# Performance work log

Hardware: AMD Instinct MI355X
Metric: run time of the kernel (lower is better)

Reference implementation:

```python
import jax, jax.numpy as jnp
import numpy as np


def setup_inputs() -> dict:
    key = jax.random.key(0)
    k1, k2 = jax.random.split(key)
    T, H, E = 16384, 4096, 8
    x = jax.random.normal(k1, (T, H), dtype=jnp.float32)
    W = jax.random.normal(k2, (E, H), dtype=jnp.float32) * 0.02  # torch Linear weight [out, in]
    return {"x": x, "W": W, "top_k": 2}


def reference(x, W, top_k):
    # router_logits = x @ W^T : [T, E]
    logits = jnp.einsum("th,eh->te", x, W)
    scores = jax.nn.softmax(logits.astype(jnp.float32), axis=-1)
    expert_weights, expert_indices = jax.lax.top_k(scores, top_k)
    return scores, expert_weights, expert_indices.astype(jnp.int32)
```

## Files before the change

### kernel.cpp

```cpp
#include <hip/hip_runtime.h>


#define ROUTER_H4 1024
#define ROUTER_E 8
#define ROWS_PER_WAVE 4
#define CHUNK 512
#define NCHUNK (ROUTER_H4 / CHUNK)

__global__ __launch_bounds__(1024) void learned_router_kernel(
    const float* __restrict__ x, const float* __restrict__ W,
    float* __restrict__ out_scores, float* __restrict__ out_w,
    float* __restrict__ out_idx, int n_rows)
{
    __shared__ float4 wlds[ROUTER_E][CHUNK];

    const int tid  = (int)threadIdx.x;
    const int wv   = tid >> 6;
    const int lane = tid & 63;
    const int row0 = (int)blockIdx.x * (16 * ROWS_PER_WAVE) + wv * ROWS_PER_WAVE;

    const float4* __restrict__ x4 = (const float4*)x;
    const float4* __restrict__ W4 = (const float4*)W;

    float acc[ROWS_PER_WAVE][ROUTER_E];
#pragma unroll
    for (int r = 0; r < ROWS_PER_WAVE; ++r)
#pragma unroll
        for (int e = 0; e < ROUTER_E; ++e) acc[r][e] = 0.f;

    for (int c = 0; c < NCHUNK; ++c) {
#pragma unroll
        for (int k = 0; k < 4; ++k) {
            const int flat = k * 1024 + tid;
            const int e    = flat >> 9;
            const int pos  = flat & (CHUNK - 1);
            wlds[e][pos] = W4[e * ROUTER_H4 + c * CHUNK + pos];
        }
        __syncthreads();

#pragma unroll 2
        for (int inner = 0; inner < CHUNK / 64; ++inner) {
            const int idx  = inner * 64 + lane;
            const int hpos = c * CHUNK + idx;
            float4 xv[ROWS_PER_WAVE];
#pragma unroll
            for (int r = 0; r < ROWS_PER_WAVE; ++r)
                xv[r] = x4[(size_t)(row0 + r) * ROUTER_H4 + hpos];
#pragma unroll
            for (int e = 0; e < ROUTER_E; ++e) {
                const float4 w4 = wlds[e][idx];
#pragma unroll
                for (int r = 0; r < ROWS_PER_WAVE; ++r)
                    acc[r][e] += xv[r].x * w4.x + xv[r].y * w4.y
                               + xv[r].z * w4.z + xv[r].w * w4.w;
            }
        }
        __syncthreads();
    }

#pragma unroll
    for (int off = 32; off > 0; off >>= 1) {
#pragma unroll
        for (int r = 0; r < ROWS_PER_WAVE; ++r)
#pragma unroll
            for (int e = 0; e < ROUTER_E; ++e)
                acc[r][e] += __shfl_xor(acc[r][e], off, 64);
    }

    if (lane == 0) {
#pragma unroll
        for (int r = 0; r < ROWS_PER_WAVE; ++r) {
            const int row = row0 + r;
            float m = acc[r][0];
#pragma unroll
            for (int e = 1; e < ROUTER_E; ++e) m = fmaxf(m, acc[r][e]);
            float p[ROUTER_E];
            float s = 0.f;
#pragma unroll
            for (int e = 0; e < ROUTER_E; ++e) { p[e] = __expf(acc[r][e] - m); s += p[e]; }
            const float inv = 1.f / s;
#pragma unroll
            for (int e = 0; e < ROUTER_E; ++e) p[e] *= inv;

            float4* os = (float4*)(out_scores + (size_t)row * ROUTER_E);
            os[0] = make_float4(p[0], p[1], p[2], p[3]);
            os[1] = make_float4(p[4], p[5], p[6], p[7]);

            int i0 = 0;
#pragma unroll
            for (int e = 1; e < ROUTER_E; ++e) if (p[e] > p[i0]) i0 = e;
            int i1 = (i0 == 0) ? 1 : 0;
#pragma unroll
            for (int e = 0; e < ROUTER_E; ++e) if (e != i0 && p[e] > p[i1]) i1 = e;

            *(float2*)(out_w + (size_t)row * 2)   = make_float2(p[i0], p[i1]);
            *(float2*)(out_idx + (size_t)row * 2) = make_float2((float)i0, (float)i1);
        }
    }
}

extern "C" void kernel_launch(void* const* d_in, const int* in_sizes, int n_in,
                              void* d_out, int out_size, void* d_ws, size_t ws_size,
                              hipStream_t stream) {
    const float* x = (const float*)d_in[0];
    const float* W = (const float*)d_in[1];
    const int T = in_sizes[0] / (ROUTER_H4 * 4);
    (void)n_in; (void)d_ws; (void)ws_size; (void)out_size;

    float* out = (float*)d_out;
    float* out_scores = out;
    float* out_w   = out + (size_t)T * ROUTER_E;
    float* out_idx = out_w + (size_t)T * 2;

    const int rows_per_block = 16 * ROWS_PER_WAVE;
    const int grid = (T + rows_per_block - 1) / rows_per_block;
    learned_router_kernel<<<grid, 1024, 0, stream>>>(x, W, out_scores, out_w, out_idx, T);
}
```

Before: 370.8 us.

## Stage full router weight in LDS once and double-buffer x loads per row pair

The kernel now loads all of W (128 KB) into shared memory in a single pass, which removes the per-chunk reload and the barriers inside the main loop. Each wave handles its four rows as two pairs. For each pair it prefetches the next group of four float4 x values while computing on the current group, a software double-buffering scheme meant to hide global-memory latency. The trade-offs are higher LDS use per block and fewer rows in flight per wave, which may lower memory-level parallelism.

Result: slower. 553.5 us (+49.3%).

```diff
diff --git a/kernel.cpp b/kernel.cpp
--- a/kernel.cpp
+++ b/kernel.cpp
@@ -3,98 +3,111 @@
 
 #define ROUTER_H4 1024
 #define ROUTER_E 8
-#define ROWS_PER_WAVE 4
-#define CHUNK 512
-#define NCHUNK (ROUTER_H4 / CHUNK)
 
 __global__ __launch_bounds__(1024) void learned_router_kernel(
     const float* __restrict__ x, const float* __restrict__ W,
     float* __restrict__ out_scores, float* __restrict__ out_w,
     float* __restrict__ out_idx, int n_rows)
 {
-    __shared__ float4 wlds[ROUTER_E][CHUNK];
+    __shared__ float4 wlds[ROUTER_E][ROUTER_H4];
 
     const int tid  = (int)threadIdx.x;
     const int wv   = tid >> 6;
     const int lane = tid & 63;
-    const int row0 = (int)blockIdx.x * (16 * ROWS_PER_WAVE) + wv * ROWS_PER_WAVE;
 
     const float4* __restrict__ x4 = (const float4*)x;
     const float4* __restrict__ W4 = (const float4*)W;
 
-    float acc[ROWS_PER_WAVE][ROUTER_E];
 #pragma unroll
-    for (int r = 0; r < ROWS_PER_WAVE; ++r)
+    for (int k = 0; k < 8; ++k) {
+        const int flat = k * 1024 + tid;
+        wlds[0][flat] = W4[flat];
+    }
+    __syncthreads();
+
+    const int rowbase = (int)blockIdx.x * 64 + wv * 4;
+
+    for (int pair = 0; pair < 2; ++pair) {
+        const int r0 = rowbase + pair * 2;
+        const float4* xr0 = x4 + (size_t)r0 * ROUTER_H4;
+        const float4* xr1 = x4 + (size_t)(r0 + 1) * ROUTER_H4;
+
+        float acc[2][ROUTER_E];
 #pragma unroll
-        for (int e = 0; e < ROUTER_E; ++e) acc[r][e] = 0.f;
+        for (int e = 0; e < ROUTER_E; ++e) { acc[0][e] = 0.f; acc[1][e] = 0.f; }
 
-    for (int c = 0; c < NCHUNK; ++c) {
+        float4 xa[2][4], xb[2][4];
 #pragma unroll
-        for (int k = 0; k < 4; ++k) {
-            const int flat = k * 1024 + tid;
-            const int e    = flat >> 9;
-            const int pos  = flat & (CHUNK - 1);
-            wlds[e][pos] = W4[e * ROUTER_H4 + c * CHUNK + pos];
+        for (int j = 0; j < 4; ++j) {
+            xa[0][j] = xr0[j * 64 + lane];
+            xa[1][j] = xr1[j * 64 + lane];
         }
-        __syncthreads();
 
-#pragma unroll 2
-        for (int inner = 0; inner < CHUNK / 64; ++inner) {
-            const int idx  = inner * 64 + lane;
-            const int hpos = c * CHUNK + idx;
-            float4 xv[ROWS_PER_WAVE];
 #pragma unroll
-            for (int r = 0; r < ROWS_PER_WAVE; ++r)
-                xv[r] = x4[(size_t)(row0 + r) * ROUTER_H4 + hpos];
+        for (int b = 0; b < 4; ++b) {
+            if (b < 3) {
 #pragma unroll
-            for (int e = 0; e < ROUTER_E; ++e) {
-                const float4 w4 = wlds[e][idx];
+                for (int j = 0; j < 4; ++j) {
+                    xb[0][j] = xr0[((b + 1) * 4 + j) * 64 + lane];
+                    xb[1][j] = xr1[((b + 1) * 4 + j) * 64 + lane];
+                }
+            }
 #pragma unroll
-                for (int r = 0; r < ROWS_PER_WAVE; ++r)
-                    acc[r][e] += xv[r].x * w4.x + xv[r].y * w4.y
-                               + xv[r].z * w4.z + xv[r].w * w4.w;
+            for (int j = 0; j < 4; ++j) {
+                const int kpos = (b * 4 + j) * 64 + lane;
+#pragma unroll
+                for (int e = 0; e < ROUTER_E; ++e) {
+                    const float4 w4 = wlds[e][kpos];
+                    acc[0][e] += xa[0][j].x * w4.x + xa[0][j].y * w4.y
+                               + xa[0][j].z * w4.z + xa[0][j].w * w4.w;
+                    acc[1][e] += xa[1][j].x * w4.x + xa[1][j].y * w4.y
+                               + xa[1][j].z * w4.z + xa[1][j].w * w4.w;
+                }
+            }
+            if (b < 3) {
+#pragma unroll
+                for (int j = 0; j < 4; ++j) { xa[0][j] = xb[0][j]; xa[1][j] = xb[1][j]; }
             }
         }
-        __syncthreads();
-    }
 
 #pragma unroll
-    for (int off = 32; off > 0; off >>= 1) {
+        for (int off = 32; off > 0; off >>= 1) {
 #pragma unroll
-        for (int r = 0; r < ROWS_PER_WAVE; ++r)
+            for (int r = 0; r < 2; ++r)
 #pragma unroll
-            for (int e = 0; e < ROUTER_E; ++e)
-                acc[r][e] += __shfl_xor(acc[r][e], off, 64);
-    }
+                for (int e = 0; e < ROUTER_E; ++e)
+                    acc[r][e] += __shfl_xor(acc[r][e], off, 64);
+        }
 
-    if (lane == 0) {
+        if (lane == 0) {
 #pragma unroll
-        for (int r = 0; r < ROWS_PER_WAVE; ++r) {
-            const int row = row0 + r;
-            float m = acc[r][0];
+            for (int r = 0; r < 2; ++r) {
+                const int row = r0 + r;
+                float m = acc[r][0];
 #pragma unroll
-            for (int e = 1; e < ROUTER_E; ++e) m = fmaxf(m, acc[r][e]);
-            float p[ROUTER_E];
-            float s = 0.f;
+                for (int e = 1; e < ROUTER_E; ++e) m = fmaxf(m, acc[r][e]);
+                float p[ROUTER_E];
+                float s = 0.f;
 #pragma unroll
-            for (int e = 0; e < ROUTER_E; ++e) { p[e] = __expf(acc[r][e] - m); s += p[e]; }
-            const float inv = 1.f / s;
+                for (int e = 0; e < ROUTER_E; ++e) { p[e] = __expf(acc[r][e] - m); s += p[e]; }
+                const float inv = 1.f / s;
 #pragma unroll
-            for (int e = 0; e < ROUTER_E; ++e) p[e] *= inv;
+                for (int e = 0; e < ROUTER_E; ++e) p[e] *= inv;
 
-            float4* os = (float4*)(out_scores + (size_t)row * ROUTER_E);
-            os[0] = make_float4(p[0], p[1], p[2], p[3]);
-            os[1] = make_float4(p[4], p[5], p[6], p[7]);
+                float4* os = (float4*)(out_scores + (size_t)row * ROUTER_E);
+                os[0] = make_float4(p[0], p[1], p[2], p[3]);
+                os[1] = make_float4(p[4], p[5], p[6], p[7]);
 
-            int i0 = 0;
+                int i0 = 0;
 #pragma unroll
-            for (int e = 1; e < ROUTER_E; ++e) if (p[e] > p[i0]) i0 = e;
-            int i1 = (i0 == 0) ? 1 : 0;
+                for (int e = 1; e < ROUTER_E; ++e) if (p[e] > p[i0]) i0 = e;
+                int i1 = (i0 == 0) ? 1 : 0;
 #pragma unroll
-            for (int e = 0; e < ROUTER_E; ++e) if (e != i0 && p[e] > p[i1]) i1 = e;
+                for (int e = 0; e < ROUTER_E; ++e) if (e != i0 && p[e] > p[i1]) i1 = e;
 
-            *(float2*)(out_w + (size_t)row * 2)   = make_float2(p[i0], p[i1]);
-            *(float2*)(out_idx + (size_t)row * 2) = make_float2((float)i0, (float)i1);
+                *(float2*)(out_w + (size_t)row * 2)   = make_float2(p[i0], p[i1]);
+                *(float2*)(out_idx + (size_t)row * 2) = make_float2((float)i0, (float)i1);
+            }
         }
     }
 }
@@ -112,7 +125,7 @@
     float* out_w   = out + (size_t)T * ROUTER_E;
     float* out_idx = out_w + (size_t)T * 2;
 
-    const int rows_per_block = 16 * ROWS_PER_WAVE;
+    const int rows_per_block = 64;
     const int grid = (T + rows_per_block - 1) / rows_per_block;
     learned_router_kernel<<<grid, 1024, 0, stream>>>(x, W, out_scores, out_w, out_idx, T);
 }
```
